# Kernel optimization log

Measured on AMD Instinct MI355X. Metric: run time of the kernel, lower is better.

The kernel has to match this reference:

```python
import jax, jax.numpy as jnp
import numpy as np

BN_EPS = 1e-5
STRIDE = 2


def setup_inputs() -> dict:
    key = jax.random.key(0)
    ks = jax.random.split(key, 8)
    B, T, Cin = 32, 1024, 128
    F, K, H = 256, 5, 512
    return {
        "x": jax.random.normal(ks[0], (B, T, Cin), jnp.float32),
        "conv_w": jax.random.normal(ks[1], (F, Cin, K), jnp.float32) * 0.05,
        "conv_b": jax.random.normal(ks[2], (F,), jnp.float32) * 0.05,
        "bn_gamma": jnp.ones((F,), jnp.float32),
        "bn_beta": jnp.zeros((F,), jnp.float32),
        "bn_mean": jnp.zeros((F,), jnp.float32),
        "bn_var": jnp.ones((F,), jnp.float32),
        "w_ih": jax.random.normal(ks[3], (4 * H, F), jnp.float32) * 0.04,
        "w_hh": jax.random.normal(ks[4], (4 * H, H), jnp.float32) * 0.04,
        "b_ih": jnp.zeros((4 * H,), jnp.float32),
        "b_hh": jnp.zeros((4 * H,), jnp.float32),
        "w_uh": jax.random.normal(ks[5], (1, H), jnp.float32) * 0.04,
        "b_uh": jnp.ones((1,), jnp.float32),
    }


def _skip_lstm(xs, w_ih, w_hh, b_ih, b_hh, w_uh, b_uh):
    # xs: [B, T', F] conv features. Skip-LSTM cell (Campos et al. Skip RNN):
    # standard LSTM + binarized state-update gate u with straight-through estimator.
    B, Tc, Fdim = xs.shape
    H = w_hh.shape[1]
    h0 = jnp.zeros((B, H), xs.dtype)
    c0 = jnp.zeros((B, H), xs.dtype)
    u0 = jnp.ones((B, 1), xs.dtype)
    # precompute input contribution to gates: [T', B, 4H]
    x_proj = jnp.einsum('btf,gf->tbg', xs, w_ih) + b_ih + b_hh

    def step(carry, xp):
        h, c, u = carry
        gates = xp + h @ w_hh.T
        i, f, g, o = jnp.split(gates, 4, axis=-1)
        c_t = jax.nn.sigmoid(f) * c + jax.nn.sigmoid(i) * jnp.tanh(g)
        h_t = jax.nn.sigmoid(o) * jnp.tanh(c_t)
        # straight-through binarization of update probability
        u_bin = u + jax.lax.stop_gradient(jnp.round(u) - u)
        c_new = u_bin * c_t + (1.0 - u_bin) * c
        h_new = u_bin * h_t + (1.0 - u_bin) * h
        du = jax.nn.sigmoid(c_new @ w_uh.T + b_uh)
        u_new = u_bin * du + (1.0 - u_bin) * (u + jnp.minimum(du, 1.0 - u))
        return (h_new, c_new, u_new), h_new

    _, hs = jax.lax.scan(step, (h0, c0, u0), x_proj)
    return jnp.swapaxes(hs, 0, 1)  # [B, T', H]


def reference(x, conv_w, conv_b, bn_gamma, bn_beta, bn_mean, bn_var,
              w_ih, w_hh, b_ih, b_hh, w_uh, b_uh):
    # Conv1d + ReLU + BatchNorm1d (eval-mode stats) on [B, Cin, T]
    xc = jnp.swapaxes(x, 1, 2)
    y = jax.lax.conv_general_dilated(
        xc, conv_w, (STRIDE,), 'VALID',
        dimension_numbers=('NCH', 'OIH', 'NCH'))
    y = jax.nn.relu(y + conv_b[None, :, None])
    inv = bn_gamma / jnp.sqrt(bn_var + BN_EPS)
    y = y * inv[None, :, None] + (bn_beta - bn_mean * inv)[None, :, None]
    y = jnp.swapaxes(y, 1, 2)  # [B, T', F]
    hs = _skip_lstm(y, w_ih, w_hh, b_ih, b_hh, w_uh, b_uh)
    return hs[:, -1, :]
```

## Files before the change

### kernel.cpp

```cpp
#include <hip/hip_runtime.h>
#include <stdint.h>
#include <math.h>

#define BB 32
#define TT 1024
#define CIN 128
#define FF 256
#define KW 5
#define HH 512
#define TP 510
#define TLAST 509
#define KC 640
#define GWG 256

#define HPK_OFF     0ull
#define PRT_OFF     131072ull
#define XP_OFF      278528ull
#define XH_OFF      (XP_OFF + 134217728ull)
#define XL_OFF      (XH_OFF + 8388608ull)
#define XSH_OFF     (XL_OFF + 8388608ull)
#define XSL_OFF     (XSH_OFF + 8388608ull)
#define WCH_OFF     (XSL_OFF + 8388608ull)
#define WCL_OFF     (WCH_OFF + 327680ull)
#define WIHH_OFF    (WCL_OFF + 327680ull)
#define WIHL_OFF    (WIHH_OFF + 1048576ull)
#define WS_NEED     (WIHL_OFF + 1048576ull)

typedef unsigned short u16;
typedef unsigned long long u64;
typedef __attribute__((ext_vector_type(8))) short short8;
typedef __attribute__((ext_vector_type(4))) float f32x4;
typedef __attribute__((ext_vector_type(4))) unsigned int u32x4;

__device__ __forceinline__ u16 f2bf(float f) {
  uint32_t u = __float_as_uint(f);
  u += 0x7fffu + ((u >> 16) & 1u);
  return (u16)(u >> 16);
}
__device__ __forceinline__ float bf2f(u16 s) { return __uint_as_float(((uint32_t)s) << 16); }
__device__ __forceinline__ void splitf(float v, u16& h, u16& l) {
  h = f2bf(v);
  l = f2bf(v - bf2f(h));
}
__device__ __forceinline__ float sigm(float x) {
  return __fdividef(1.f, 1.f + __expf(-x));
}
__device__ __forceinline__ float tanh_fast(float x) {
  float xc = fminf(x, 20.f);
  float e = __expf(2.f * xc);
  return (e - 1.f) * __fdividef(1.f, e + 1.f);
}

__global__ void prep_kernel(const float* __restrict__ x, const float* __restrict__ conv_w,
                            const float* __restrict__ w_ih,
                            u16* __restrict__ xh, u16* __restrict__ xl,
                            u16* __restrict__ wch, u16* __restrict__ wcl,
                            u16* __restrict__ wihh, u16* __restrict__ wihl) {
  int i = blockIdx.x * 256 + threadIdx.x;
  if (i < 4194304) {
    u16 h, l; splitf(x[i], h, l); xh[i] = h; xl[i] = l;
  } else if (i < 4194304 + 163840) {
    int j = i - 4194304;
    int f = j / 640, kk = j % 640;
    int c = kk & 127, k = kk >> 7;
    u16 h, l; splitf(conv_w[f * 640 + c * 5 + k], h, l);
    wch[f * 640 + kk] = h; wcl[f * 640 + kk] = l;
  } else if (i < 4194304 + 163840 + 524288) {
    int j = i - (4194304 + 163840);
    u16 h, l; splitf(w_ih[j], h, l); wihh[j] = h; wihl[j] = l;
  }
}

template <int MODE>
__global__ __launch_bounds__(256, 1) void gemm_kernel(
    const u16* __restrict__ Ah, const u16* __restrict__ Al,
    const u16* __restrict__ Bh, const u16* __restrict__ Bl,
    const float* __restrict__ e0, const float* __restrict__ e1,
    const float* __restrict__ e2, const float* __restrict__ e3, const float* __restrict__ e4,
    u16* __restrict__ outh, u16* __restrict__ outl, float* __restrict__ outf) {
  const int KDIM = (MODE == 0) ? KC : 256;
  const int MT   = (MODE == 0) ? 2 : 16;
  int bx = blockIdx.x;
  int m0 = (bx % MT) * 128;
  int n0 = (bx / MT) * 128;
  __shared__ __attribute__((aligned(16))) u16 lds[4][4096];
  int t = threadIdx.x;
  int wave = t >> 6, lane = t & 63;
  int wm = wave & 1, wn = wave >> 1;

  f32x4 acc[4][4];
#pragma unroll
  for (int i = 0; i < 4; i++)
#pragma unroll
    for (int j = 0; j < 4; j++) acc[i][j] = (f32x4){0.f, 0.f, 0.f, 0.f};

  for (int k0 = 0; k0 < KDIM; k0 += 32) {
    __syncthreads();
#pragma unroll
    for (int half = 0; half < 2; half++) {
      int e = half * 256 + t;
      int l = e & 63, tile = e >> 6;
      int kk = k0 + ((l >> 4) * 8);
      {
        int row = m0 + tile * 16 + (l & 15);
        const u16* sh = Ah + (long)row * KDIM + kk;
        const u16* sl = Al + (long)row * KDIM + kk;
        *(short8*)&lds[0][e * 8] = *(const short8*)sh;
        *(short8*)&lds[1][e * 8] = *(const short8*)sl;
      }
      {
        int n = n0 + tile * 16 + (l & 15);
        long base;
        if (MODE == 0) {
          int tp = n >> 5; if (tp > TLAST) tp = TLAST;
          base = (long)(n & 31) * 131072 + (long)tp * 256;
        } else {
          base = (long)n * 256;
        }
        *(short8*)&lds[2][e * 8] = *(const short8*)(Bh + base + kk);
        *(short8*)&lds[3][e * 8] = *(const short8*)(Bl + base + kk);
      }
    }
    __syncthreads();
    short8 af[4][2], bf[4][2];
#pragma unroll
    for (int i = 0; i < 4; i++) {
      af[i][0] = *(const short8*)&lds[0][((wm * 4 + i) * 64 + lane) * 8];
      af[i][1] = *(const short8*)&lds[1][((wm * 4 + i) * 64 + lane) * 8];
      bf[i][0] = *(const short8*)&lds[2][((wn * 4 + i) * 64 + lane) * 8];
      bf[i][1] = *(const short8*)&lds[3][((wn * 4 + i) * 64 + lane) * 8];
    }
#pragma unroll
    for (int am = 0; am < 4; am++)
#pragma unroll
      for (int an = 0; an < 4; an++) {
        acc[am][an] = __builtin_amdgcn_mfma_f32_16x16x32_bf16(af[am][0], bf[an][0], acc[am][an], 0, 0, 0);
        acc[am][an] = __builtin_amdgcn_mfma_f32_16x16x32_bf16(af[am][0], bf[an][1], acc[am][an], 0, 0, 0);
        acc[am][an] = __builtin_amdgcn_mfma_f32_16x16x32_bf16(af[am][1], bf[an][0], acc[am][an], 0, 0, 0);
      }
  }
#pragma unroll
  for (int am = 0; am < 4; am++)
#pragma unroll
    for (int an = 0; an < 4; an++) {
      int n = n0 + (wn * 4 + an) * 16 + (lane & 15);
#pragma unroll
      for (int r = 0; r < 4; r++) {
        int m = m0 + (wm * 4 + am) * 16 + (lane >> 4) * 4 + r;
        float v = acc[am][an][r];
        if (MODE == 0) {
          float inv = e1[m] / sqrtf(e4[m] + 1e-5f);
          float sh  = e2[m] - e3[m] * inv;
          v = fmaxf(v + e0[m], 0.f) * inv + sh;
          u16 h, l; splitf(v, h, l);
          outh[(long)n * 256 + m] = h;
          outl[(long)n * 256 + m] = l;
        } else {
          v += e0[m] + e1[m];
          int tp = n >> 5, b = n & 31;
          int grp = b >> 2, bb = b & 3;
          int q = m >> 9, unit = m & 511;
          int sl = unit >> 4, jjj = unit & 15;
          outf[(((long)grp * 512 + tp) * 32 + sl) * 256 + q * 64 + jjj * 4 + bb] = v;
        }
      }
    }
}

__global__ __launch_bounds__(256, 1) void scan_kernel(
    const float* __restrict__ xpg,
    const float* __restrict__ w_hh,
    const float* __restrict__ w_uh,
    const float* __restrict__ b_uh_p,
    uint32_t* __restrict__ hpk,
    u64* __restrict__ prt,
    float* __restrict__ outp)
{
  __shared__ __attribute__((aligned(16))) u16 sh_hi[4 * 528];
  __shared__ __attribute__((aligned(16))) u16 sh_lo[4 * 528];
  __shared__ float gpart[4][4][16][4];
  __shared__ float sparts[4][32];
  __shared__ float u_l[4], ubin_l[4];
  __shared__ float wuh_l[16];
  int group = blockIdx.x & 7, slot = blockIdx.x >> 3;
  int t = threadIdx.x;
  int wave = t >> 6, lane = t & 63;
  int um = lane & 15, kq = lane >> 4;
  int nbc = um & 3;

  if (t < 16) wuh_l[t] = w_uh[slot * 16 + t];
  if (t < 4)  { u_l[t] = 1.0f; ubin_l[t] = 1.0f; }

  short8 wfh[4][4], wfl[4][4];
#pragma unroll
  for (int q = 0; q < 4; q++) {
    long row = (long)(q * 512 + slot * 16 + um) * 512;
#pragma unroll
    for (int k4 = 0; k4 < 4; k4++) {
      union { short8 v; u16 u[8]; } Uh, Ul;
      long col0 = wave * 128 + k4 * 32 + kq * 8;
#pragma unroll
      for (int i = 0; i < 8; i++) splitf(w_hh[row + col0 + i], Uh.u[i], Ul.u[i]);
      wfh[q][k4] = Uh.v; wfl[q][k4] = Ul.v;
    }
  }
  float bu = b_uh_p[0];

  int jj = t & 15, bbt = t >> 4;
  float c_reg = 0.f, h_reg = 0.f;

  uint32_t* hgrp = hpk + (long)group * 4096;
  u64*      pgrp = prt + (long)group * 256;

  __syncthreads();

  for (int s = 0; s < TP; s++) {
    int par = s & 1, np = par ^ 1;
    f32x4 xq;
    if (t < 64) {
      const float* xb = xpg + (((long)group * 512 + s) * 32 + slot) * 256;
      float x0 = xb[0 * 64 + jj * 4 + bbt];
      float x1 = xb[1 * 64 + jj * 4 + bbt];
      float x2 = xb[2 * 64 + jj * 4 + bbt];
      float x3 = xb[3 * 64 + jj * 4 + bbt];
      xq = (f32x4){x0, x1, x2, x3};
    }
    int b = t >> 6, u0 = (t & 63) * 8;
    if (s == 0) {
      *(u32x4*)&sh_hi[b * 528 + u0] = (u32x4){0u, 0u, 0u, 0u};
      *(u32x4*)&sh_lo[b * 528 + u0] = (u32x4){0u, 0u, 0u, 0u};
    } else {
      int pslot = (t & 63) >> 1;
      const u64* pw = pgrp + (long)par * 128 + b * 32 + pslot;
      u64 w;
      do {
        w = __hip_atomic_load(pw, __ATOMIC_RELAXED, __HIP_MEMORY_SCOPE_AGENT);
      } while ((uint32_t)(w >> 32) != (uint32_t)s);
      if ((t & 1) == 0) sparts[b][pslot] = __uint_as_float((uint32_t)w);
      const u64* hp = (const u64*)(hgrp + (long)par * 2048 + b * 512 + u0);
      u64 v0 = __hip_atomic_load(hp,     __ATOMIC_RELAXED, __HIP_MEMORY_SCOPE_AGENT);
      u64 v1 = __hip_atomic_load(hp + 1, __ATOMIC_RELAXED, __HIP_MEMORY_SCOPE_AGENT);
      u64 v2 = __hip_atomic_load(hp + 2, __ATOMIC_RELAXED, __HIP_MEMORY_SCOPE_AGENT);
      u64 v3 = __hip_atomic_load(hp + 3, __ATOMIC_RELAXED, __HIP_MEMORY_SCOPE_AGENT);
      uint32_t p[8] = {(uint32_t)v0, (uint32_t)(v0 >> 32), (uint32_t)v1, (uint32_t)(v1 >> 32),
                       (uint32_t)v2, (uint32_t)(v2 >> 32), (uint32_t)v3, (uint32_t)(v3 >> 32)};
      u32x4 hv, lv;
#pragma unroll
      for (int r = 0; r < 4; r++) {
        hv[r] = __builtin_amdgcn_perm(p[2 * r + 1], p[2 * r], 0x07060302u);
        lv[r] = __builtin_amdgcn_perm(p[2 * r + 1], p[2 * r], 0x05040100u);
      }
      *(u32x4*)&sh_hi[b * 528 + u0] = hv;
      *(u32x4*)&sh_lo[b * 528 + u0] = lv;
    }
    __syncthreads();
    if (s > 0 && t < 4) {
      float a = 0.f;
#pragma unroll
      for (int i = 0; i < 32; i++) a += sparts[t][i];
      float du = sigm(a + bu);
      float up = u_l[t], ubp = ubin_l[t];
      float un = (ubp > 0.5f) ? du : (up + fminf(du, 1.f - up));
      u_l[t] = un; ubin_l[t] = rintf(un);
    }
    f32x4 A0[4], A1[4], A2[4];
#pragma unroll
    for (int q = 0; q < 4; q++) {
      A0[q] = (f32x4){0.f, 0.f, 0.f, 0.f}; A1[q] = A0[q]; A2[q] = A0[q];
    }
#pragma unroll
    for (int k4 = 0; k4 < 4; k4++) {
      int ko = (wave * 4 + k4) * 32 + kq * 8;
      short8 bh = *(const short8*)&sh_hi[nbc * 528 + ko];
      short8 bl = *(const short8*)&sh_lo[nbc * 528 + ko];
#pragma unroll
      for (int q = 0; q < 4; q++) {
        A0[q] = __builtin_amdgcn_mfma_f32_16x16x32_bf16(wfh[q][k4], bh, A0[q], 0, 0, 0);
        A1[q] = __builtin_amdgcn_mfma_f32_16x16x32_bf16(wfh[q][k4], bl, A1[q], 0, 0, 0);
        A2[q] = __builtin_amdgcn_mfma_f32_16x16x32_bf16(wfl[q][k4], bh, A2[q], 0, 0, 0);
      }
    }
    if (um < 4) {
#pragma unroll
      for (int q = 0; q < 4; q++)
#pragma unroll
        for (int r = 0; r < 4; r++)
          gpart[wave][q][kq * 4 + r][um] = (A0[q][r] + A1[q][r]) + A2[q][r];
    }
    __syncthreads();
    if (t < 64) {
      float g[4];
#pragma unroll
      for (int q = 0; q < 4; q++) {
        float a = xq[q];
#pragma unroll
        for (int w = 0; w < 4; w++) a += gpart[w][q][jj][bbt];
        g[q] = a;
      }
      float ig = sigm(g[0]), fg = sigm(g[1]), og = sigm(g[3]);
      float gt = tanh_fast(g[2]);
      float ct = fg * c_reg + ig * gt;
      float ht = og * tanh_fast(ct);
      bool upd = ubin_l[bbt] > 0.5f;
      float cn = upd ? ct : c_reg;
      float hn = upd ? ht : h_reg;
      c_reg = cn; h_reg = hn;
      u16 hhi, hlo; splitf(hn, hhi, hlo);
      uint32_t pk = ((uint32_t)hhi << 16) | (uint32_t)hlo;
      __hip_atomic_store(hgrp + (long)np * 2048 + bbt * 512 + slot * 16 + jj, pk,
                         __ATOMIC_RELAXED, __HIP_MEMORY_SCOPE_AGENT);
      float pr = cn * wuh_l[jj];
      pr += __shfl_xor(pr, 1); pr += __shfl_xor(pr, 2);
      pr += __shfl_xor(pr, 4); pr += __shfl_xor(pr, 8);
      if (s == TLAST) outp[(long)(group * 4 + bbt) * 512 + slot * 16 + jj] = hn;
      __threadfence_block();
      if ((t & 15) == 0) {
        u64 pw = ((u64)(uint32_t)(s + 1) << 32) | (u64)__float_as_uint(pr);
        __hip_atomic_store(pgrp + (long)np * 128 + bbt * 32 + slot, pw,
                           __ATOMIC_RELAXED, __HIP_MEMORY_SCOPE_AGENT);
      }
    }
  }
}

extern "C" void kernel_launch(void* const* d_in, const int* in_sizes, int n_in,
                              void* d_out, int out_size, void* d_ws, size_t ws_size,
                              hipStream_t stream) {
  const float* x      = (const float*)d_in[0];
  const float* conv_w = (const float*)d_in[1];
  const float* conv_b = (const float*)d_in[2];
  const float* gamma  = (const float*)d_in[3];
  const float* beta   = (const float*)d_in[4];
  const float* mean   = (const float*)d_in[5];
  const float* var    = (const float*)d_in[6];
  const float* w_ih   = (const float*)d_in[7];
  const float* w_hh   = (const float*)d_in[8];
  const float* b_ih   = (const float*)d_in[9];
  const float* b_hh   = (const float*)d_in[10];
  const float* w_uh   = (const float*)d_in[11];
  const float* b_uh   = (const float*)d_in[12];
  float* out = (float*)d_out;

  if (ws_size < WS_NEED) return;

  char* w = (char*)d_ws;
  uint32_t* hpk = (uint32_t*)(w + HPK_OFF);
  u64*   prt   = (u64*)(w + PRT_OFF);
  float* xp    = (float*)(w + XP_OFF);
  u16*   xh    = (u16*)(w + XH_OFF);
  u16*   xl    = (u16*)(w + XL_OFF);
  u16*   xsh   = (u16*)(w + XSH_OFF);
  u16*   xsl   = (u16*)(w + XSL_OFF);
  u16*   wch   = (u16*)(w + WCH_OFF);
  u16*   wcl   = (u16*)(w + WCL_OFF);
  u16*   wihh  = (u16*)(w + WIHH_OFF);
  u16*   wihl  = (u16*)(w + WIHL_OFF);


  prep_kernel<<<19072, 256, 0, stream>>>(x, conv_w, w_ih, xh, xl, wch, wcl, wihh, wihl);

  gemm_kernel<0><<<2 * 128, 256, 0, stream>>>(wch, wcl, xh, xl,
                                              conv_b, gamma, beta, mean, var,
                                              xsh, xsl, nullptr);
  gemm_kernel<1><<<16 * 128, 256, 0, stream>>>(wihh, wihl, xsh, xsl,
                                               b_ih, b_hh, nullptr, nullptr, nullptr,
                                               nullptr, nullptr, xp);
  scan_kernel<<<GWG, 256, 0, stream>>>(xp, w_hh, w_uh, b_uh, hpk, prt, out);
}
```

Measured before the change: 2.123 ms.

## Tag hidden-state words with step counter to poll data directly

```diff
diff --git a/kernel.cpp b/kernel.cpp
--- a/kernel.cpp
+++ b/kernel.cpp
@@ -14,7 +14,7 @@
 #define GWG 256
 
 #define HPK_OFF     0ull
-#define PRT_OFF     131072ull
+#define PRT_OFF     262144ull
 #define XP_OFF      278528ull
 #define XH_OFF      (XP_OFF + 134217728ull)
 #define XL_OFF      (XH_OFF + 8388608ull)
@@ -172,7 +172,7 @@
     const float* __restrict__ w_hh,
     const float* __restrict__ w_uh,
     const float* __restrict__ b_uh_p,
-    uint32_t* __restrict__ hpk,
+    u64* __restrict__ hpk,
     u64* __restrict__ prt,
     float* __restrict__ outp)
 {
@@ -209,8 +209,8 @@
   int jj = t & 15, bbt = t >> 4;
   float c_reg = 0.f, h_reg = 0.f;
 
-  uint32_t* hgrp = hpk + (long)group * 4096;
-  u64*      pgrp = prt + (long)group * 256;
+  u64* hgrp = hpk + (long)group * 4096;
+  u64* pgrp = prt + (long)group * 256;
 
   __syncthreads();
 
@@ -232,18 +232,33 @@
     } else {
       int pslot = (t & 63) >> 1;
       const u64* pw = pgrp + (long)par * 128 + b * 32 + pslot;
-      u64 w;
-      do {
-        w = __hip_atomic_load(pw, __ATOMIC_RELAXED, __HIP_MEMORY_SCOPE_AGENT);
-      } while ((uint32_t)(w >> 32) != (uint32_t)s);
-      if ((t & 1) == 0) sparts[b][pslot] = __uint_as_float((uint32_t)w);
-      const u64* hp = (const u64*)(hgrp + (long)par * 2048 + b * 512 + u0);
-      u64 v0 = __hip_atomic_load(hp,     __ATOMIC_RELAXED, __HIP_MEMORY_SCOPE_AGENT);
-      u64 v1 = __hip_atomic_load(hp + 1, __ATOMIC_RELAXED, __HIP_MEMORY_SCOPE_AGENT);
-      u64 v2 = __hip_atomic_load(hp + 2, __ATOMIC_RELAXED, __HIP_MEMORY_SCOPE_AGENT);
-      u64 v3 = __hip_atomic_load(hp + 3, __ATOMIC_RELAXED, __HIP_MEMORY_SCOPE_AGENT);
-      uint32_t p[8] = {(uint32_t)v0, (uint32_t)(v0 >> 32), (uint32_t)v1, (uint32_t)(v1 >> 32),
-                       (uint32_t)v2, (uint32_t)(v2 >> 32), (uint32_t)v3, (uint32_t)(v3 >> 32)};
+      const u64* hp = hgrp + (long)par * 2048 + b * 512 + u0;
+      bool needp = ((t & 1) == 0);
+      u64 v0, v1, v2, v3, v4, v5, v6, v7, wv = 0;
+      uint32_t tg = (uint32_t)s;
+      for (;;) {
+        v0 = __hip_atomic_load(hp + 0, __ATOMIC_RELAXED, __HIP_MEMORY_SCOPE_AGENT);
+        v1 = __hip_atomic_load(hp + 1, __ATOMIC_RELAXED, __HIP_MEMORY_SCOPE_AGENT);
+        v2 = __hip_atomic_load(hp + 2, __ATOMIC_RELAXED, __HIP_MEMORY_SCOPE_AGENT);
+        v3 = __hip_atomic_load(hp + 3, __ATOMIC_RELAXED, __HIP_MEMORY_SCOPE_AGENT);
+        v4 = __hip_atomic_load(hp + 4, __ATOMIC_RELAXED, __HIP_MEMORY_SCOPE_AGENT);
+        v5 = __hip_atomic_load(hp + 5, __ATOMIC_RELAXED, __HIP_MEMORY_SCOPE_AGENT);
+        v6 = __hip_atomic_load(hp + 6, __ATOMIC_RELAXED, __HIP_MEMORY_SCOPE_AGENT);
+        v7 = __hip_atomic_load(hp + 7, __ATOMIC_RELAXED, __HIP_MEMORY_SCOPE_AGENT);
+        bool ok = ((uint32_t)(v0 >> 32) == tg) & ((uint32_t)(v1 >> 32) == tg) &
+                  ((uint32_t)(v2 >> 32) == tg) & ((uint32_t)(v3 >> 32) == tg) &
+                  ((uint32_t)(v4 >> 32) == tg) & ((uint32_t)(v5 >> 32) == tg) &
+                  ((uint32_t)(v6 >> 32) == tg) & ((uint32_t)(v7 >> 32) == tg);
+        if (needp) {
+          wv = __hip_atomic_load(pw, __ATOMIC_RELAXED, __HIP_MEMORY_SCOPE_AGENT);
+          ok &= ((uint32_t)(wv >> 32) == tg);
+        }
+        if (ok) break;
+        __builtin_amdgcn_s_sleep(1);
+      }
+      if (needp) sparts[b][pslot] = __uint_as_float((uint32_t)wv);
+      uint32_t p[8] = {(uint32_t)v0, (uint32_t)v1, (uint32_t)v2, (uint32_t)v3,
+                       (uint32_t)v4, (uint32_t)v5, (uint32_t)v6, (uint32_t)v7};
       u32x4 hv, lv;
 #pragma unroll
       for (int r = 0; r < 4; r++) {
@@ -289,6 +304,7 @@
     }
     __syncthreads();
     if (t < 64) {
+      __builtin_amdgcn_s_setprio(1);
       float g[4];
 #pragma unroll
       for (int q = 0; q < 4; q++) {
@@ -307,18 +323,19 @@
       c_reg = cn; h_reg = hn;
       u16 hhi, hlo; splitf(hn, hhi, hlo);
       uint32_t pk = ((uint32_t)hhi << 16) | (uint32_t)hlo;
-      __hip_atomic_store(hgrp + (long)np * 2048 + bbt * 512 + slot * 16 + jj, pk,
+      u64 hw = ((u64)(uint32_t)(s + 1) << 32) | (u64)pk;
+      __hip_atomic_store(hgrp + (long)np * 2048 + bbt * 512 + slot * 16 + jj, hw,
                          __ATOMIC_RELAXED, __HIP_MEMORY_SCOPE_AGENT);
       float pr = cn * wuh_l[jj];
       pr += __shfl_xor(pr, 1); pr += __shfl_xor(pr, 2);
       pr += __shfl_xor(pr, 4); pr += __shfl_xor(pr, 8);
       if (s == TLAST) outp[(long)(group * 4 + bbt) * 512 + slot * 16 + jj] = hn;
-      __threadfence_block();
       if ((t & 15) == 0) {
-        u64 pw = ((u64)(uint32_t)(s + 1) << 32) | (u64)__float_as_uint(pr);
-        __hip_atomic_store(pgrp + (long)np * 128 + bbt * 32 + slot, pw,
+        u64 pwv = ((u64)(uint32_t)(s + 1) << 32) | (u64)__float_as_uint(pr);
+        __hip_atomic_store(pgrp + (long)np * 128 + bbt * 32 + slot, pwv,
                            __ATOMIC_RELAXED, __HIP_MEMORY_SCOPE_AGENT);
       }
+      __builtin_amdgcn_s_setprio(0);
     }
   }
 }
@@ -344,7 +361,7 @@
   if (ws_size < WS_NEED) return;
 
   char* w = (char*)d_ws;
-  uint32_t* hpk = (uint32_t*)(w + HPK_OFF);
+  u64*   hpk   = (u64*)(w + HPK_OFF);
   u64*   prt   = (u64*)(w + PRT_OFF);
   float* xp    = (float*)(w + XP_OFF);
   u16*   xh    = (u16*)(w + XH_OFF);
```

Result: slower. 2.610 ms (+22.9%).
